# Kernel optimization log

Hardware: AMD Instinct MI355X
Metric: run time of the kernel (lower is better)

The kernel has to match this reference:

```python
import jax, jax.numpy as jnp
import numpy as np

B, N, E, L, G, F, H = 64, 500, 16000, 64, 64, 8, 128

def setup_inputs() -> dict:
    key = jax.random.key(0)
    ks = jax.random.split(key, 8)
    return {
        "x": jax.random.normal(ks[0], (B, N, L), dtype=jnp.float32),
        "incidence": jax.random.normal(ks[1], (N, E), dtype=jnp.float32),
        "ef": jax.random.normal(ks[2], (E, F), dtype=jnp.float32),
        "W1": jax.random.normal(ks[3], (F, H), dtype=jnp.float32) * 0.1,
        "b1": jax.random.normal(ks[4], (H,), dtype=jnp.float32) * 0.1,
        "W2": jax.random.normal(ks[5], (H, L * G), dtype=jnp.float32) * 0.1,
        "b2": jax.random.normal(ks[6], (L * G,), dtype=jnp.float32) * 0.1,
        "b_gc": jax.random.normal(ks[7], (G,), dtype=jnp.float32) * 0.1,
    }

def reference(x, incidence, ef, W1, b1, W2, b2, b_gc):
    # MLP-generated per-edge kernel: [E, G, L]
    h = jax.nn.relu(ef @ W1 + b1)
    kernel = (h @ W2 + b2).reshape(E, G, L)
    # gather node features onto edges: [B, E, L]
    t = jnp.einsum('bnl,ne->bel', x, incidence)
    # per-edge batched matvec: [B, E, G]
    y = jnp.einsum('egl,bel->beg', kernel, t)
    # scatter back to nodes: [B, N, G]
    y = jnp.einsum('ne,beg->bng', incidence, y)
    # gc is a frozen identity Linear -> just add bias, then ReLU
    y = jax.nn.relu(y + b_gc)
    return y.reshape(x.shape[0], -1)
```

## Files before the change

kernel.cpp:

```cpp
#include <hip/hip_runtime.h>

constexpr int B_ = 64, N_ = 500, E_ = 16000, L_ = 64, G_ = 64, F_ = 8, H_ = 128;
constexpr int GL_ = 4096;
constexpr int NP_ = 512;
constexpr int KS_ = 4;
constexpr int ACC_ELEMS = B_ * N_ * G_;

using bf16x8  = __attribute__((ext_vector_type(8))) short;
using f32x4   = __attribute__((ext_vector_type(4))) float;
using ushort8 = __attribute__((ext_vector_type(8))) unsigned short;

#define MFMA16(a, b, c) __builtin_amdgcn_mfma_f32_16x16x32_bf16((a), (b), (c), 0, 0, 0)

typedef __attribute__((address_space(3))) unsigned int       lds_u32;
typedef const __attribute__((address_space(1))) unsigned int glb_u32;

static __device__ __forceinline__ unsigned short f2bf(float f) {
    union { float f; unsigned u; } v; v.f = f;
    unsigned r = v.u + 0x7fffu + ((v.u >> 16) & 1u);
    return (unsigned short)(r >> 16);
}
static __device__ __forceinline__ float bf2f(unsigned short s) {
    union { float f; unsigned u; } v; v.u = ((unsigned)s) << 16;
    return v.f;
}

static __device__ __forceinline__ void stage_tile(
    const unsigned short* __restrict__ g, int ld, int r0, int kk,
    unsigned short* lds, int tid)
{
    #pragma unroll
    for (int c = 0; c < 4; ++c) {
        const int ch  = tid + c * 256;
        const int row = ch >> 3, off = (ch & 7) * 8;
        __builtin_amdgcn_global_load_lds(
            (glb_u32*)(g + (size_t)(r0 + row) * ld + kk + off),
            (lds_u32*)(lds + (size_t)ch * 8), 16, 0, 0);
    }
}

template<int MODE>
__global__ __launch_bounds__(256)
void gemm128(const unsigned short* __restrict__ A, int lda,
             const unsigned short* __restrict__ Bm, int ldb,
             int K, int nN,
             unsigned short* __restrict__ C, int ldc,
             const float* __restrict__ bias)
{
    const int nwg = gridDim.x;
    const int bid = blockIdx.x;
    const int swz = (nwg & 7) ? bid : ((bid & 7) * (nwg >> 3) + (bid >> 3));
    const int m0 = (swz / nN) * 128, n0 = (swz % nN) * 128;

    const int tid  = threadIdx.x;
    const int lane = tid & 63, wid = tid >> 6;
    const int wm = wid >> 1, wn = wid & 1;
    const int fr = lane & 15, fq = lane >> 4;

    __shared__ __align__(16) unsigned short smem[2 * 128 * 64];
    unsigned short* As = smem;
    unsigned short* Bs = smem + 128 * 64;

    const f32x4 fz = {0.f, 0.f, 0.f, 0.f};
    f32x4 acc[4][4] = {{fz, fz, fz, fz}, {fz, fz, fz, fz},
                       {fz, fz, fz, fz}, {fz, fz, fz, fz}};

    const int nk = K / 64;
    for (int kt = 0; kt < nk; ++kt) {
        stage_tile(A, lda, m0, kt * 64, As, tid);
        stage_tile(Bm, ldb, n0, kt * 64, Bs, tid);
        __syncthreads();
        #pragma unroll
        for (int ks = 0; ks < 2; ++ks) {
            bf16x8 af[4], bf[4];
            #pragma unroll
            for (int i = 0; i < 4; ++i)
                af[i] = *(const bf16x8*)&As[(wm * 64 + i * 16 + fr) * 64 + ks * 32 + fq * 8];
            #pragma unroll
            for (int j = 0; j < 4; ++j)
                bf[j] = *(const bf16x8*)&Bs[(wn * 64 + j * 16 + fr) * 64 + ks * 32 + fq * 8];
            #pragma unroll
            for (int i = 0; i < 4; ++i)
                #pragma unroll
                for (int j = 0; j < 4; ++j)
                    acc[i][j] = MFMA16(af[i], bf[j], acc[i][j]);
        }
        __syncthreads();
    }

    auto Cs = (unsigned short(*)[128])smem;
    #pragma unroll
    for (int i = 0; i < 4; ++i)
        #pragma unroll
        for (int j = 0; j < 4; ++j) {
            float bv = 0.f;
            if constexpr (MODE == 1) bv = bias[n0 + wn * 64 + j * 16 + fr];
            #pragma unroll
            for (int r = 0; r < 4; ++r)
                Cs[wm * 64 + i * 16 + fq * 4 + r][wn * 64 + j * 16 + fr] =
                    f2bf(acc[i][j][r] + bv);
        }
    __syncthreads();
    const int r2 = tid >> 4, o2 = (tid & 15) * 8;
    #pragma unroll
    for (int i = 0; i < 8; ++i) {
        const int row = i * 16 + r2;
        *(uint4*)&C[(size_t)(m0 + row) * ldc + n0 + o2] = *(const uint4*)&Cs[row][o2];
    }
}

__global__ __launch_bounds__(512)
void k_y8(unsigned short* tc, const unsigned short* __restrict__ Kc)
{
    const int e0 = blockIdx.x * 8;
    const int tid = threadIdx.x, lane = tid & 63, w = tid >> 6;
    const int e = e0 + w;
    const int fr = lane & 15, fq = lane >> 4;
    const unsigned short* A  = &tc[(size_t)e * GL_];
    const unsigned short* Bp = &Kc[(size_t)e * GL_];
    const f32x4 fz = {0.f, 0.f, 0.f, 0.f};
    f32x4 acc[4][4] = {{fz, fz, fz, fz}, {fz, fz, fz, fz},
                       {fz, fz, fz, fz}, {fz, fz, fz, fz}};
    #pragma unroll
    for (int ks = 0; ks < 2; ++ks) {
        bf16x8 af[4], bf[4];
        #pragma unroll
        for (int i = 0; i < 4; ++i)
            af[i] = *(const bf16x8*)&A[(i * 16 + fr) * 64 + ks * 32 + fq * 8];
        #pragma unroll
        for (int j = 0; j < 4; ++j)
            bf[j] = *(const bf16x8*)&Bp[(j * 16 + fr) * 64 + ks * 32 + fq * 8];
        #pragma unroll
        for (int i = 0; i < 4; ++i)
            #pragma unroll
            for (int j = 0; j < 4; ++j)
                acc[i][j] = MFMA16(af[i], bf[j], acc[i][j]);
    }
    __shared__ unsigned short y8[GL_ * 8];
    #pragma unroll
    for (int i = 0; i < 4; ++i)
        #pragma unroll
        for (int j = 0; j < 4; ++j)
            #pragma unroll
            for (int r = 0; r < 4; ++r) {
                const int bg = (i * 16 + fq * 4 + r) * 64 + j * 16 + fr;
                y8[bg * 8 + w] = f2bf(acc[i][j][r]);
            }
    __syncthreads();
    unsigned short* dst = tc + (size_t)e0 * GL_;
    #pragma unroll
    for (int p = 0; p < 8; ++p) {
        const int o = (p * 512 + tid) * 8;
        *(uint4*)&dst[o] = *(const uint4*)&y8[o];
    }
}

__global__ __launch_bounds__(256)
void k_accd(const unsigned short* __restrict__ Ae,
            const unsigned short* __restrict__ y8,
            unsigned short* __restrict__ planesB, int pbase, int K)
{
    const int xcd = blockIdx.x & 7, grp = blockIdx.x >> 3;
    const int m0 = (grp & 7) * 64;
    const int n0 = (xcd + 8 * (grp >> 3)) * 128;
    const int KSY = gridDim.y;
    const int kl = ((K / KSY) / 64) * 64;
    const int kbeg = blockIdx.y * kl;
    const int kend = ((int)blockIdx.y == KSY - 1) ? K : kbeg + kl;

    const int lane = threadIdx.x & 63, wid = threadIdx.x >> 6;
    const int wm = wid >> 1, wn = wid & 1;
    const int fr = lane & 15, fq = lane >> 4;

    const f32x4 fz = {0.f, 0.f, 0.f, 0.f};
    f32x4 acc[2][4] = {{fz, fz, fz, fz}, {fz, fz, fz, fz}};

    for (int kk = kbeg; kk < kend; kk += 64) {
        #pragma unroll
        for (int ks = 0; ks < 2; ++ks) {
            const int e8 = kk + ks * 32 + fq * 8;
            const size_t eb = (size_t)(e8 >> 3);
            bf16x8 af[2], bf[4];
            #pragma unroll
            for (int i = 0; i < 2; ++i)
                af[i] = *(const bf16x8*)&Ae[(eb * NP_ + m0 + wm * 32 + i * 16 + fr) * 8];
            #pragma unroll
            for (int j = 0; j < 4; ++j)
                bf[j] = *(const bf16x8*)&y8[eb * GL_ * 8 + (n0 + wn * 64 + j * 16 + fr) * 8];
            #pragma unroll
            for (int i = 0; i < 2; ++i)
                #pragma unroll
                for (int j = 0; j < 4; ++j)
                    acc[i][j] = MFMA16(af[i], bf[j], acc[i][j]);
        }
    }

    unsigned short* pl = planesB + (size_t)(pbase + blockIdx.y) * ACC_ELEMS;
    #pragma unroll
    for (int i = 0; i < 2; ++i)
        #pragma unroll
        for (int j = 0; j < 4; ++j) {
            const int col = n0 + wn * 64 + j * 16 + fr;
            const int b = col >> 6, g = col & 63;
            #pragma unroll
            for (int r = 0; r < 4; ++r) {
                const int n = m0 + wm * 32 + i * 16 + fq * 4 + r;
                if (n < N_)
                    pl[((size_t)b * N_ + n) * G_ + g] = f2bf(acc[i][j][r]);
            }
        }
}

__global__ __launch_bounds__(256)
void k_cvt_incB8(const float* __restrict__ inc, unsigned short* __restrict__ incB8)
{
    const int e0 = blockIdx.x * 64;
    const int n0 = blockIdx.y * 64;
    const int tid = threadIdx.x;
    __shared__ unsigned short sm[64][72];
    const int cl = tid & 63;
    for (int rr = tid >> 6; rr < 64; rr += 4) {
        const int n = n0 + rr;
        sm[rr][cl] = (n < N_) ? f2bf(inc[(size_t)n * E_ + e0 + cl]) : (unsigned short)0;
    }
    __syncthreads();
    const int eb = tid >> 5, idx = tid & 31;
    #pragma unroll
    for (int k = 0; k < 2; ++k) {
        const int row = idx * 2 + k;
        *(ushort8*)&incB8[((size_t)((e0 >> 3) + eb) * NP_ + n0 + row) * 8] =
            *(const ushort8*)&sm[row][eb * 8];
    }
}

__global__ __launch_bounds__(256)
void k_tr32(const float* __restrict__ in, unsigned short* __restrict__ out,
            int R, int C, int Rp, size_t inZ, size_t outZ)
{
    in  += (size_t)blockIdx.z * inZ;
    out += (size_t)blockIdx.z * outZ;
    const int c0 = blockIdx.x * 64, r0 = blockIdx.y * 64;
    __shared__ float sm[64][65];
    const int cl = threadIdx.x & 63;
    for (int rr = threadIdx.x >> 6; rr < 64; rr += 4) {
        const int r = r0 + rr;
        sm[cl][rr] = (r < R) ? in[(size_t)r * C + c0 + cl] : 0.f;
    }
    __syncthreads();
    const int cw = threadIdx.x >> 2, j0 = (threadIdx.x & 3) * 16;
    unsigned short tmp[16];
    #pragma unroll
    for (int j = 0; j < 16; ++j) tmp[j] = f2bf(sm[cw][j0 + j]);
    *(ushort8*)&out[(size_t)(c0 + cw) * Rp + r0 + j0]     = *(ushort8*)&tmp[0];
    *(ushort8*)&out[(size_t)(c0 + cw) * Rp + r0 + j0 + 8] = *(ushort8*)&tmp[8];
}

__global__ __launch_bounds__(256)
void k_h(const float* __restrict__ ef, const float* __restrict__ W1,
         const float* __restrict__ b1, unsigned short* __restrict__ h)
{
    const int idx = blockIdx.x * 256 + threadIdx.x;
    const int e = idx >> 7, hh = idx & 127;
    float v = b1[hh];
    const float* efp = &ef[(size_t)e * F_];
    #pragma unroll
    for (int f = 0; f < F_; ++f) v += efp[f] * W1[f * H_ + hh];
    h[idx] = f2bf(fmaxf(v, 0.f));
}

__global__ __launch_bounds__(256)
void k_final(const unsigned short* __restrict__ planesB, int P,
             const float* __restrict__ bgc, float* __restrict__ out)
{
    const int i = (blockIdx.x * 256 + threadIdx.x) * 8;
    if (i >= ACC_ELEMS) return;
    float s[8];
    #pragma unroll
    for (int j = 0; j < 8; ++j) s[j] = bgc[(i + j) & 63];
    for (int p = 0; p < P; ++p) {
        const ushort8 v = *(const ushort8*)&planesB[(size_t)p * ACC_ELEMS + i];
        #pragma unroll
        for (int j = 0; j < 8; ++j) s[j] += bf2f((unsigned short)v[j]);
    }
    float4 o0, o1;
    o0.x = fmaxf(s[0], 0.f); o0.y = fmaxf(s[1], 0.f);
    o0.z = fmaxf(s[2], 0.f); o0.w = fmaxf(s[3], 0.f);
    o1.x = fmaxf(s[4], 0.f); o1.y = fmaxf(s[5], 0.f);
    o1.z = fmaxf(s[6], 0.f); o1.w = fmaxf(s[7], 0.f);
    *(float4*)&out[i]     = o0;
    *(float4*)&out[i + 4] = o1;
}

extern "C" void kernel_launch(void* const* d_in, const int* in_sizes, int n_in,
                              void* d_out, int out_size, void* d_ws, size_t ws_size,
                              hipStream_t stream) {
    const float* x   = (const float*)d_in[0];
    const float* inc = (const float*)d_in[1];
    const float* ef  = (const float*)d_in[2];
    const float* W1  = (const float*)d_in[3];
    const float* b1  = (const float*)d_in[4];
    const float* W2  = (const float*)d_in[5];
    const float* b2  = (const float*)d_in[6];
    const float* bgc = (const float*)d_in[7];
    float* out = (float*)d_out;

    const size_t persistU16 = (size_t)NP_ * E_
                            + (size_t)E_ * NP_
                            + (size_t)B_ * L_ * NP_
                            + (size_t)E_ * H_
                            + (size_t)GL_ * H_;
    const size_t persistBytes = persistU16 * 2;

    int nc = 1, Ec = E_;
    for (; nc <= 16; ++nc) {
        Ec = ((E_ + nc - 1) / nc + 127) / 128 * 128;
        const size_t need = persistBytes
                          + (size_t)nc * KS_ * ACC_ELEMS * 2
                          + 2 * (size_t)Ec * GL_ * 2;
        if (need <= ws_size) break;
    }
    if (nc > 16) { nc = 16; Ec = 1024; }

    unsigned short* planesB = (unsigned short*)d_ws;
    unsigned short* incB8 = planesB + (size_t)nc * KS_ * ACC_ELEMS;
    unsigned short* incT = incB8 + (size_t)NP_ * E_;
    unsigned short* xT   = incT + (size_t)E_ * NP_;
    unsigned short* h    = xT   + (size_t)B_ * L_ * NP_;
    unsigned short* W2T  = h    + (size_t)E_ * H_;
    unsigned short* Kc   = W2T  + (size_t)GL_ * H_;
    unsigned short* tc   = Kc   + (size_t)Ec * GL_;

    k_cvt_incB8<<<dim3(E_ / 64, NP_ / 64), 256, 0, stream>>>(inc, incB8);
    k_tr32<<<dim3(E_ / 64, NP_ / 64, 1), 256, 0, stream>>>(inc, incT, N_, E_, NP_, 0, 0);
    k_tr32<<<dim3(1, NP_ / 64, B_),      256, 0, stream>>>(x, xT, N_, L_, NP_,
                                                           (size_t)N_ * L_, (size_t)L_ * NP_);
    k_tr32<<<dim3(GL_ / 64, H_ / 64, 1), 256, 0, stream>>>(W2, W2T, H_, GL_, H_, 0, 0);
    k_h<<<dim3(E_ * H_ / 256), 256, 0, stream>>>(ef, W1, b1, h);

    int cidx = 0;
    for (int e_off = 0; e_off < E_; e_off += Ec, ++cidx) {
        const int ec = (E_ - e_off) < Ec ? (E_ - e_off) : Ec;
        gemm128<1><<<dim3((ec / 128) * 32), 256, 0, stream>>>(
            h + (size_t)e_off * H_, H_, W2T, H_, H_, 32, Kc, GL_, b2);
        gemm128<0><<<dim3((ec / 128) * 32), 256, 0, stream>>>(
            incT + (size_t)e_off * NP_, NP_, xT, NP_, NP_, 32, tc, GL_, nullptr);
        k_y8<<<dim3(ec / 8), 512, 0, stream>>>(tc, Kc);
        k_accd<<<dim3(256, KS_), 256, 0, stream>>>(
            incB8 + (size_t)e_off * NP_, tc, planesB, cidx * KS_, ec);
    }

    k_final<<<dim3(ACC_ELEMS / 2048), 256, 0, stream>>>(planesB, nc * KS_, bgc, out);
}
```

Measured before the change: 409.3 us.

## XOR-swizzle GEMM LDS tiles and merge the two per-chunk GEMMs into one launch

The LDS staging of each 128x64 bf16 tile now XOR-swizzles the 16-byte chunk index with the row, and the fragment reads apply the same swizzle. This is meant to remove LDS bank conflicts on the strided row reads. Separately, the kernel-generation GEMM and the gather GEMM are fused into a single launch that uses blockIdx.y to pick the operand set. That saves one launch per chunk and lets the two GEMMs overlap on the GPU, at the cost of a runtime bias branch instead of a template specialization.

```diff
diff --git a/kernel.cpp b/kernel.cpp
--- a/kernel.cpp
+++ b/kernel.cpp
@@ -32,20 +32,20 @@
     #pragma unroll
     for (int c = 0; c < 4; ++c) {
         const int ch  = tid + c * 256;
-        const int row = ch >> 3, off = (ch & 7) * 8;
+        const int row = ch >> 3;
+        const int csw = (ch & 7) ^ (row & 7);
         __builtin_amdgcn_global_load_lds(
-            (glb_u32*)(g + (size_t)(r0 + row) * ld + kk + off),
+            (glb_u32*)(g + (size_t)(r0 + row) * ld + kk + csw * 8),
             (lds_u32*)(lds + (size_t)ch * 8), 16, 0, 0);
     }
 }
 
-template<int MODE>
-__global__ __launch_bounds__(256)
-void gemm128(const unsigned short* __restrict__ A, int lda,
-             const unsigned short* __restrict__ Bm, int ldb,
-             int K, int nN,
-             unsigned short* __restrict__ C, int ldc,
-             const float* __restrict__ bias)
+static __device__ __forceinline__ void gemm_body(
+    const unsigned short* __restrict__ A, int lda,
+    const unsigned short* __restrict__ Bm, int ldb,
+    int K, int nN,
+    unsigned short* __restrict__ C, int ldc,
+    const float* __restrict__ bias)
 {
     const int nwg = gridDim.x;
     const int bid = blockIdx.x;
@@ -64,6 +64,11 @@
     const f32x4 fz = {0.f, 0.f, 0.f, 0.f};
     f32x4 acc[4][4] = {{fz, fz, fz, fz}, {fz, fz, fz, fz},
                        {fz, fz, fz, fz}, {fz, fz, fz, fz}};
+
+    const int rowA[4] = {wm * 64 + 0 * 16 + fr, wm * 64 + 1 * 16 + fr,
+                         wm * 64 + 2 * 16 + fr, wm * 64 + 3 * 16 + fr};
+    const int rowB[4] = {wn * 64 + 0 * 16 + fr, wn * 64 + 1 * 16 + fr,
+                         wn * 64 + 2 * 16 + fr, wn * 64 + 3 * 16 + fr};
 
     const int nk = K / 64;
     for (int kt = 0; kt < nk; ++kt) {
@@ -75,10 +80,12 @@
             bf16x8 af[4], bf[4];
             #pragma unroll
             for (int i = 0; i < 4; ++i)
-                af[i] = *(const bf16x8*)&As[(wm * 64 + i * 16 + fr) * 64 + ks * 32 + fq * 8];
+                af[i] = *(const bf16x8*)&As[rowA[i] * 64 +
+                         (((ks * 4 + fq) ^ (rowA[i] & 7)) * 8)];
             #pragma unroll
             for (int j = 0; j < 4; ++j)
-                bf[j] = *(const bf16x8*)&Bs[(wn * 64 + j * 16 + fr) * 64 + ks * 32 + fq * 8];
+                bf[j] = *(const bf16x8*)&Bs[rowB[j] * 64 +
+                         (((ks * 4 + fq) ^ (rowB[j] & 7)) * 8)];
             #pragma unroll
             for (int i = 0; i < 4; ++i)
                 #pragma unroll
@@ -93,8 +100,7 @@
     for (int i = 0; i < 4; ++i)
         #pragma unroll
         for (int j = 0; j < 4; ++j) {
-            float bv = 0.f;
-            if constexpr (MODE == 1) bv = bias[n0 + wn * 64 + j * 16 + fr];
+            const float bv = bias ? bias[n0 + wn * 64 + j * 16 + fr] : 0.f;
             #pragma unroll
             for (int r = 0; r < 4; ++r)
                 Cs[wm * 64 + i * 16 + fq * 4 + r][wn * 64 + j * 16 + fr] =
@@ -107,6 +113,20 @@
         const int row = i * 16 + r2;
         *(uint4*)&C[(size_t)(m0 + row) * ldc + n0 + o2] = *(const uint4*)&Cs[row][o2];
     }
+}
+
+__global__ __launch_bounds__(256)
+void gemm_pair(const unsigned short* __restrict__ A0, int lda0,
+               const unsigned short* __restrict__ B0, int ldb0, int K0,
+               unsigned short* __restrict__ C0, const float* __restrict__ bias0,
+               const unsigned short* __restrict__ A1, int lda1,
+               const unsigned short* __restrict__ B1, int ldb1, int K1,
+               unsigned short* __restrict__ C1, int nN)
+{
+    if (blockIdx.y == 0)
+        gemm_body(A0, lda0, B0, ldb0, K0, nN, C0, GL_, bias0);
+    else
+        gemm_body(A1, lda1, B1, ldb1, K1, nN, C1, GL_, nullptr);
 }
 
 __global__ __launch_bounds__(512)
@@ -340,10 +360,9 @@
     int cidx = 0;
     for (int e_off = 0; e_off < E_; e_off += Ec, ++cidx) {
         const int ec = (E_ - e_off) < Ec ? (E_ - e_off) : Ec;
-        gemm128<1><<<dim3((ec / 128) * 32), 256, 0, stream>>>(
-            h + (size_t)e_off * H_, H_, W2T, H_, H_, 32, Kc, GL_, b2);
-        gemm128<0><<<dim3((ec / 128) * 32), 256, 0, stream>>>(
-            incT + (size_t)e_off * NP_, NP_, xT, NP_, NP_, 32, tc, GL_, nullptr);
+        gemm_pair<<<dim3((ec / 128) * 32, 2), 256, 0, stream>>>(
+            h + (size_t)e_off * H_, H_, W2T, H_, H_, Kc, b2,
+            incT + (size_t)e_off * NP_, NP_, xT, NP_, NP_, tc, 32);
         k_y8<<<dim3(ec / 8), 512, 0, stream>>>(tc, Kc);
         k_accd<<<dim3(256, KS_), 256, 0, stream>>>(
             incB8 + (size_t)e_off * NP_, tc, planesB, cidx * KS_, ec);
```

Result: faster. 397.5 us (-2.9%).
